# Kernel tuning notes

Hardware: AMD Instinct MI355X
Metric: run time of the kernel (lower is better)

## Reference

```python
import jax, jax.numpy as jnp
import numpy as np
from jax import lax

B, C, H, W = 64, 512, 20, 15
N = H * W  # must be 300 (ChannelAttention dim)
EPS = 1e-5


def layernorm(x, w, b):
    m = x.mean(-1, keepdims=True)
    v = x.var(-1, keepdims=True)
    return (x - m) * lax.rsqrt(v + EPS) * w + b


def batchnorm(x, w, b):  # training-mode BN over (B,H,W), x: (B,C,H,W)
    m = x.mean((0, 2, 3), keepdims=True)
    v = x.var((0, 2, 3), keepdims=True)
    return (x - m) * lax.rsqrt(v + EPS) * w[None, :, None, None] + b[None, :, None, None]


def cross_linear_attn(x1, x2, kv1_w, kv2_w, heads):
    # x: (B, n, c); kv_w: (2c, c). Linear-attention variant: softmax over channel axis of k^T v.
    b, n, c = x1.shape
    d = c // heads
    scale = d ** -0.5

    def split_q(x):
        return x.reshape(b, n, heads, d).transpose(0, 2, 1, 3)  # (b,h,n,d)

    def kv(x, w):
        t = (x @ w.T).reshape(b, n, 2, heads, d).transpose(2, 0, 3, 1, 4)
        return t[0], t[1]  # each (b,h,n,d)

    q1, q2 = split_q(x1), split_q(x2)
    k1, v1 = kv(x1, kv1_w)
    k2, v2 = kv(x2, kv2_w)

    def ctx(k, v):  # (b,h,d,d), softmax over dim -2
        return jax.nn.softmax(jnp.einsum('bhnd,bhne->bhde', k, v) * scale, axis=-2)

    c1, c2 = ctx(k1, v1), ctx(k2, v2)

    def out(q, cx):
        return jnp.einsum('bhnd,bhde->bhne', q, cx).transpose(0, 2, 1, 3).reshape(b, n, c)

    return out(q1, c2), out(q2, c1)  # cross: q1 uses ctx2, q2 uses ctx1


def conv1x1(x, w):  # x: (B,Ci,H,W), w: (Co,Ci)
    return jnp.einsum('oi,bihw->bohw', w, x)


def setup_inputs() -> dict:
    key = jax.random.key(0)
    ks = jax.random.split(key, 24)
    g = lambda i, shape, s=0.02: jax.random.normal(ks[i], shape, jnp.float32) * s
    inp = {
        'x1': jax.random.normal(ks[0], (B, C, H, W), jnp.float32),
        'x2': jax.random.normal(ks[1], (B, C, H, W), jnp.float32),
        # CrossPath channel_proj1/2: Linear(C, 2C) + LayerNorm(2C)
        'cp1_w': g(2, (2 * C, C)), 'cp1_b': jnp.zeros((2 * C,), jnp.float32),
        'ln1_w': jnp.ones((2 * C,), jnp.float32), 'ln1_b': jnp.zeros((2 * C,), jnp.float32),
        'cp2_w': g(3, (2 * C, C)), 'cp2_b': jnp.zeros((2 * C,), jnp.float32),
        'ln2_w': jnp.ones((2 * C,), jnp.float32), 'ln2_b': jnp.zeros((2 * C,), jnp.float32),
        # SpatialAttention (dim=C, heads=8) kv linears, no bias
        's_kv1_w': g(4, (2 * C, C)), 's_kv2_w': g(5, (2 * C, C)),
        # ChannelAttention (dim=N=300, heads=4) kv linears, no bias
        'c_kv1_w': g(6, (2 * N, N)), 'c_kv2_w': g(7, (2 * N, N)),
        # ChannelEmbed(2C -> C)
        'res_w': g(8, (C, 2 * C), np.sqrt(2.0 / C)),
        'ce1_w': g(9, (C, 2 * C), np.sqrt(2.0 / C)), 'ce1_b': jnp.zeros((C,), jnp.float32),
        'dw_w': g(10, (C, 1, 3, 3), np.sqrt(2.0 / 9.0)), 'dw_b': jnp.zeros((C,), jnp.float32),
        'ce3_w': g(11, (C, C), np.sqrt(2.0 / C)), 'ce3_b': jnp.zeros((C,), jnp.float32),
        'bn_e_w': jnp.ones((C,), jnp.float32), 'bn_e_b': jnp.zeros((C,), jnp.float32),
        'bn_o_w': jnp.ones((C,), jnp.float32), 'bn_o_b': jnp.zeros((C,), jnp.float32),
    }
    return inp


def reference(x1, x2, cp1_w, cp1_b, ln1_w, ln1_b, cp2_w, cp2_b, ln2_w, ln2_b,
              s_kv1_w, s_kv2_w, c_kv1_w, c_kv2_w,
              res_w, ce1_w, ce1_b, dw_w, dw_b, ce3_w, ce3_b,
              bn_e_w, bn_e_b, bn_o_w, bn_o_b):
    b, c, h, w = x1.shape
    n = h * w
    t1 = x1.reshape(b, c, n).transpose(0, 2, 1)  # (B,N,C)
    t2 = x2.reshape(b, c, n).transpose(0, 2, 1)

    a1 = jax.nn.relu(layernorm(t1 @ cp1_w.T + cp1_b, ln1_w, ln1_b))
    a2 = jax.nn.relu(layernorm(t2 @ cp2_w.T + cp2_b, ln2_w, ln2_b))
    c1, s1 = a1[..., :c], a1[..., c:]
    c2, s2 = a2[..., :c], a2[..., c:]

    v1, v2 = cross_linear_attn(s1, s2, s_kv1_w, s_kv2_w, heads=8)
    z1, z2 = cross_linear_attn(c1.transpose(0, 2, 1), c2.transpose(0, 2, 1),
                               c_kv1_w, c_kv2_w, heads=4)
    s = v1 + v2                                  # (B,N,C)
    cc = (z1 + z2).transpose(0, 2, 1)            # (B,N,C)

    merge = jnp.concatenate([s, cc], axis=-1)    # (B,N,2C)
    xm = merge.transpose(0, 2, 1).reshape(b, 2 * c, h, w)

    residual = conv1x1(xm, res_w)
    e = conv1x1(xm, ce1_w) + ce1_b[None, :, None, None]
    e = lax.conv_general_dilated(e, dw_w, (1, 1), 'SAME',
                                 dimension_numbers=('NCHW', 'OIHW', 'NCHW'),
                                 feature_group_count=c) + dw_b[None, :, None, None]
    e = jnp.where(e >= 0, e, 0.01 * e)  # LeakyReLU(0.01)
    e = conv1x1(e, ce3_w) + ce3_b[None, :, None, None]
    e = batchnorm(e, bn_e_w, bn_e_b)
    return batchnorm(residual + e, bn_o_w, bn_o_b)
```

## Files before the change

kernel.cpp:

```cpp
#include <hip/hip_runtime.h>

typedef unsigned short u16;
typedef __attribute__((ext_vector_type(8))) short bh8;
typedef __attribute__((ext_vector_type(4))) float f4;

__device__ __forceinline__ u16 f2b(float f){
  unsigned int u = __float_as_uint(f);
  u += 0x7fffu + ((u >> 16) & 1u);
  return (u16)(u >> 16);
}
__device__ __forceinline__ float b2f(u16 h){
  return __uint_as_float(((unsigned int)h) << 16);
}
__device__ __forceinline__ void gl16(const u16* g, u16* l){
  __builtin_amdgcn_global_load_lds((const __attribute__((address_space(1))) void*)g,
                                   (__attribute__((address_space(3))) void*)l, 16, 0, 0);
}

__global__ void pack_plain(const float* __restrict__ src, u16* __restrict__ dst, int count){
  int i = blockIdx.x*256 + threadIdx.x;
  if (i < count) dst[i] = f2b(src[i]);
}
__global__ void pack_ckv_k(const float* __restrict__ src, u16* __restrict__ dst){
  int i = blockIdx.x*256 + threadIdx.x;
  int nn = i / 320, kk = i - (i/320)*320;
  int t_ = (nn >= 320) ? 1 : 0;
  int rem = nn - t_*320;
  int hh = rem / 80, dd = rem - hh*80;
  int kh = kk / 80, kd = kk - kh*80;
  float v = 0.f;
  if (dd < 75 && kd < 75)
    v = src[(size_t)(t_*300 + hh*75 + dd)*300 + (kh*75 + kd)];
  dst[i] = f2b(v);
}
__global__ void pack_dw(const float* __restrict__ src, u16* __restrict__ dst){
  int i = blockIdx.x*256 + threadIdx.x;
  if (i < 4608){
    int t = i >> 9, c = i & 511;
    dst[i] = f2b(src[c*9 + t]);
  }
}
__global__ void pad_zero(u16* __restrict__ slack){
  const int j = blockIdx.x*256 + threadIdx.x;
  if (j < 2048) slack[j] = 0;
}

__global__ __launch_bounds__(256)
void transpose_k(const float* __restrict__ x, u16* __restrict__ t)
{
  __shared__ float tile[32][33];
  const int n0 = blockIdx.x * 32, c0 = blockIdx.y * 32, b = blockIdx.z;
  const int ln = threadIdx.x & 31, lr = threadIdx.x >> 5;
  #pragma unroll
  for (int q = 0; q < 4; q++) {
    const int c = c0 + lr + q*8, n = n0 + ln;
    tile[lr + q*8][ln] = (n < 300) ? x[((long)b*512 + c)*300 + n] : 0.f;
  }
  __syncthreads();
  #pragma unroll
  for (int q = 0; q < 4; q++) {
    const int n = n0 + lr + q*8;
    if (n < 300) t[((long)b*300 + n)*512 + c0 + ln] = f2b(tile[ln][lr + q*8]);
  }
}

template<int OUTF, int HASB>
__global__ __launch_bounds__(256)
void gemm_k(const u16* __restrict__ A, int lda,
            const u16* __restrict__ Bw, int ldb,
            u16* __restrict__ Cb, float* __restrict__ Cf, int ldc,
            const float* __restrict__ bias, int K)
{
  __shared__ u16 As[2][4096];
  __shared__ u16 Bs[2][4096];
  const int tid = threadIdx.x;
  const int gx = gridDim.x;
  const int nwg = gx * gridDim.y;
  const int flat = blockIdx.y * gx + blockIdx.x;
  const int newid = (flat & 7) * (nwg >> 3) + (flat >> 3);
  const long n0 = (long)(newid % gx) * 128;
  const long m0 = (long)(newid / gx) * 128;
  const int wave = tid >> 6, lane = tid & 63;
  const int l15 = lane & 15, lg = lane >> 4;
  const int wr = (wave >> 1) * 64, wc = (wave & 1) * 64;
  const int arow = tid >> 2;
  const int aseg = (((tid & 3) ^ ((arow >> 1) & 3))) * 8;
  const u16* Ag0 = A + (m0 + arow) * (long)lda + aseg;
  const u16* Ag1 = Ag0 + 64L * lda;
  const u16* Bg0 = Bw + (n0 + arow) * (long)ldb + aseg;
  const u16* Bg1 = Bg0 + 64L * ldb;
  const int to8 = tid * 8;
  int roA[4], roB[4];
  #pragma unroll
  for (int i = 0; i < 4; i++){
    const int rA = wr + i*16 + l15;
    roA[i] = rA*32 + ((lg ^ ((rA >> 1) & 3)) * 8);
    const int rB = wc + i*16 + l15;
    roB[i] = rB*32 + ((lg ^ ((rB >> 1) & 3)) * 8);
  }
  f4 acc[4][4] = {};
  const int NT = K >> 5;
  gl16(Ag0, &As[0][to8]); gl16(Ag1, &As[0][2048 + to8]);
  gl16(Bg0, &Bs[0][to8]); gl16(Bg1, &Bs[0][2048 + to8]);
  __syncthreads();
  int cur = 0;
  for (int t = 0; t < NT - 1; t++) {
    const int kt = (t + 1) << 5;
    const int nb = cur ^ 1;
    gl16(Ag0 + kt, &As[nb][to8]); gl16(Ag1 + kt, &As[nb][2048 + to8]);
    gl16(Bg0 + kt, &Bs[nb][to8]); gl16(Bg1 + kt, &Bs[nb][2048 + to8]);
    bh8 af[4], bf[4];
    #pragma unroll
    for (int mi = 0; mi < 4; mi++) af[mi] = *(const bh8*)&As[cur][roA[mi]];
    #pragma unroll
    for (int ni = 0; ni < 4; ni++) bf[ni] = *(const bh8*)&Bs[cur][roB[ni]];
    #pragma unroll
    for (int mi = 0; mi < 4; mi++)
      #pragma unroll
      for (int ni = 0; ni < 4; ni++)
        acc[mi][ni] = __builtin_amdgcn_mfma_f32_16x16x32_bf16(af[mi], bf[ni], acc[mi][ni], 0, 0, 0);
    __syncthreads();
    cur = nb;
  }
  {
    bh8 af[4], bf[4];
    #pragma unroll
    for (int mi = 0; mi < 4; mi++) af[mi] = *(const bh8*)&As[cur][roA[mi]];
    #pragma unroll
    for (int ni = 0; ni < 4; ni++) bf[ni] = *(const bh8*)&Bs[cur][roB[ni]];
    #pragma unroll
    for (int mi = 0; mi < 4; mi++)
      #pragma unroll
      for (int ni = 0; ni < 4; ni++)
        acc[mi][ni] = __builtin_amdgcn_mfma_f32_16x16x32_bf16(af[mi], bf[ni], acc[mi][ni], 0, 0, 0);
  }
  if (OUTF == 2) {
    if (n0 < 512) {
      #pragma unroll
      for (int ni = 0; ni < 4; ni++) {
        const long cn = n0 + wc + ni*16 + l15;
        #pragma unroll
        for (int mi = 0; mi < 4; mi++)
          #pragma unroll
          for (int r = 0; r < 4; r++) {
            const long cm = m0 + wr + mi*16 + lg*4 + r;
            Cf[cm * ldc + cn] = acc[mi][ni][r];
          }
      }
    } else {
      #pragma unroll
      for (int ni = 0; ni < 4; ni++) {
        const long cn = n0 - 512 + wc + ni*16 + l15;
        const float bv = bias[cn];
        #pragma unroll
        for (int mi = 0; mi < 4; mi++)
          #pragma unroll
          for (int r = 0; r < 4; r++) {
            const long cm = m0 + wr + mi*16 + lg*4 + r;
            Cb[cm * ldc + cn] = f2b(acc[mi][ni][r] + bv);
          }
      }
    }
  } else {
    #pragma unroll
    for (int ni = 0; ni < 4; ni++) {
      const long cn = n0 + wc + ni*16 + l15;
      const float bv = HASB ? bias[cn] : 0.0f;
      #pragma unroll
      for (int mi = 0; mi < 4; mi++) {
        #pragma unroll
        for (int r = 0; r < 4; r++) {
          const long cm = m0 + wr + mi*16 + lg*4 + r;
          const float v = acc[mi][ni][r] + bv;
          if (OUTF) Cf[cm * ldc + cn] = v;
          else      Cb[cm * ldc + cn] = f2b(v);
        }
      }
    }
  }
}

__global__ __launch_bounds__(256)
void ln_kernel(const u16* __restrict__ apre, const float* __restrict__ lw, const float* __restrict__ lb,
               u16* __restrict__ s, u16* __restrict__ cT)
{
  __shared__ u16 tile[40][520];
  const int bh = blockIdx.x;
  const int b = bh >> 2, h = bh & 3;
  const int z = blockIdx.y;
  const int dd0 = z ? 40 : 0;
  const int ndd = z ? 35 : 40;
  const int segbase = z ? 5 : 0;
  const int tid = threadIdx.x, w = tid >> 6, lane = tid & 63;
  const int r0 = b*300 + h*75 + dd0;
  for (int dl = w; dl < ndd; dl += 4){
    const int r = r0 + dl;
    const u16* row = apre + (size_t)r*1024 + lane*8;
    const bh8 vc = *(const bh8*)row;
    const bh8 vs = *(const bh8*)(row + 512);
    float fc[8], fs[8];
    float sm = 0.f, sq = 0.f;
    #pragma unroll
    for (int j = 0; j < 8; j++){
      fc[j] = b2f((u16)vc[j]); fs[j] = b2f((u16)vs[j]);
      sm += fc[j] + fs[j];
      sq += fc[j]*fc[j] + fs[j]*fs[j];
    }
    #pragma unroll
    for (int o = 32; o; o >>= 1){ sm += __shfl_xor(sm, o); sq += __shfl_xor(sq, o); }
    const float mean = sm * (1.f/1024.f);
    const float rstd = rsqrtf(sq*(1.f/1024.f) - mean*mean + 1e-5f);
    bh8 oc, os;
    #pragma unroll
    for (int j = 0; j < 8; j++){
      const int c = lane*8 + j;
      const float y1 = (fc[j]-mean)*rstd*lw[c] + lb[c];
      oc[j] = (short)f2b(fmaxf(y1, 0.f));
      const float y2 = (fs[j]-mean)*rstd*lw[512+c] + lb[512+c];
      os[j] = (short)f2b(fmaxf(y2, 0.f));
    }
    *(bh8*)&tile[dl][lane*8] = oc;
    *(bh8*)&s[(size_t)r*512 + lane*8] = os;
  }
  __syncthreads();
  for (int i = tid; i < 2560; i += 256){
    const int c = i / 5, sg = i - (i/5)*5;
    const int seg = segbase + sg;
    bh8 ov;
    #pragma unroll
    for (int j = 0; j < 8; j++){
      const int dl = seg*8 + j - dd0;
      ov[j] = (short)((dl >= 0 && dl < ndd) ? tile[dl][c] : (u16)0);
    }
    *(bh8*)&cT[((size_t)b*512 + c)*320 + h*80 + seg*8] = ov;
  }
}

template<int D, int DREAL, int OS>
__global__ __launch_bounds__(256)
void ctx_kernel(const u16* __restrict__ kva, const u16* __restrict__ kvb,
                u16* __restrict__ outp, int K, int RS, int VOFF, float scale)
{
  constexpr int NT = D/16, MT = D/16, MTL = (MT+3)/4, SEG = D/8;
  __shared__ u16 vT[D][40];
  __shared__ u16 kT[D][40];
  const int h = blockIdx.x, b = blockIdx.y, iq = blockIdx.z;
  const int Hn = gridDim.x;
  const u16* base = (iq ? kvb : kva) + (size_t)b*K*RS + h*D;
  u16* out = outp + (((size_t)iq*64 + b)*Hn + h)*(size_t)(D*OS);
  const int tid = threadIdx.x, w = tid >> 6, lane = tid & 63, l15 = lane & 15, lg = lane >> 4;
  f4 acc[MTL][NT] = {};
  for (int k0 = 0; k0 < K; k0 += 32) {
    __syncthreads();
    for (int sI = tid; sI < 32*SEG; sI += 256) {
      const int nn = sI / SEG, dseg = sI - (sI/SEG)*SEG;
      bh8 kk = {}, vv = {};
      const int krow = k0 + nn;
      if (krow < K) {
        const u16* p = base + (size_t)krow*RS + dseg*8;
        kk = *(const bh8*)p;
        vv = *(const bh8*)(p + VOFF);
      }
      #pragma unroll
      for (int j = 0; j < 8; j++){
        kT[dseg*8+j][nn] = (u16)kk[j];
        vT[dseg*8+j][nn] = (u16)vv[j];
      }
    }
    __syncthreads();
    #pragma unroll
    for (int ii = 0; ii < MTL; ii++){
      const int mt = w + ii*4;
      if (MT % 4 != 0 && mt >= MT) break;
      const bh8 a = *(const bh8*)&vT[mt*16 + l15][lg*8];
      #pragma unroll
      for (int nt = 0; nt < NT; nt++){
        const bh8 bb = *(const bh8*)&kT[nt*16 + l15][lg*8];
        acc[ii][nt] = __builtin_amdgcn_mfma_f32_16x16x32_bf16(a, bb, acc[ii][nt], 0, 0, 0);
      }
    }
  }
  #pragma unroll
  for (int ii = 0; ii < MTL; ii++){
    const int mt = w + ii*4;
    if (MT % 4 != 0 && mt >= MT) continue;
    #pragma unroll
    for (int r = 0; r < 4; r++){
      const int e = mt*16 + lg*4 + r;
      float xs[NT]; float mx = -1e30f;
      #pragma unroll
      for (int nt = 0; nt < NT; nt++){
        float x = acc[ii][nt][r] * scale;
        if (DREAL != D && (nt*16 + l15) >= DREAL) x = -1e30f;
        xs[nt] = x; mx = fmaxf(mx, x);
      }
      mx = fmaxf(mx, __shfl_xor(mx,1)); mx = fmaxf(mx, __shfl_xor(mx,2));
      mx = fmaxf(mx, __shfl_xor(mx,4)); mx = fmaxf(mx, __shfl_xor(mx,8));
      float smv = 0.f;
      #pragma unroll
      for (int nt = 0; nt < NT; nt++){
        const float p = (xs[nt] > -1e29f) ? __expf(xs[nt]-mx) : 0.f;
        xs[nt] = p; smv += p;
      }
      smv += __shfl_xor(smv,1); smv += __shfl_xor(smv,2);
      smv += __shfl_xor(smv,4); smv += __shfl_xor(smv,8);
      const float inv = 1.f / smv;
      #pragma unroll
      for (int nt = 0; nt < NT; nt++)
        out[(size_t)e*OS + nt*16 + l15] = f2b(xs[nt]*inv);
      if (OS > D) out[(size_t)e*OS + D + l15] = 0;
    }
  }
}

__global__ __launch_bounds__(256)
void sp_out_kernel(const u16* __restrict__ s1, const u16* __restrict__ s2,
                   const u16* __restrict__ csT, u16* __restrict__ merge)
{
  const int h = blockIdx.x, b = blockIdx.y;
  const int tid = threadIdx.x, w = tid >> 6, lane = tid & 63, l15 = lane & 15, lg = lane >> 4;
  const u16* c1 = csT + (((size_t)b)*8 + h)*4096;
  const u16* c2 = csT + (((size_t)64 + b)*8 + h)*4096;
  for (int mt = w; mt < 19; mt += 4) {
    const int m = mt*16 + l15;
    const bool mv = (m < 300);
    const u16* q1 = s1 + ((size_t)b*300 + m)*512 + h*64;
    const u16* q2 = s2 + ((size_t)b*300 + m)*512 + h*64;
    f4 acc[4] = {};
    #pragma unroll
    for (int kc = 0; kc < 2; kc++){
      bh8 a1 = {}, a2 = {};
      if (mv){ a1 = *(const bh8*)(q1 + kc*32 + lg*8); a2 = *(const bh8*)(q2 + kc*32 + lg*8); }
      #pragma unroll
      for (int nt = 0; nt < 4; nt++){
        const bh8 b2v = *(const bh8*)&c2[(size_t)(nt*16+l15)*64 + kc*32 + lg*8];
        acc[nt] = __builtin_amdgcn_mfma_f32_16x16x32_bf16(a1, b2v, acc[nt], 0, 0, 0);
        const bh8 b1v = *(const bh8*)&c1[(size_t)(nt*16+l15)*64 + kc*32 + lg*8];
        acc[nt] = __builtin_amdgcn_mfma_f32_16x16x32_bf16(a2, b1v, acc[nt], 0, 0, 0);
      }
    }
    #pragma unroll
    for (int nt = 0; nt < 4; nt++)
      #pragma unroll
      for (int r = 0; r < 4; r++){
        const int mm = mt*16 + lg*4 + r;
        if (mm < 300)
          merge[((size_t)b*300 + mm)*1024 + h*64 + nt*16 + l15] = f2b(acc[nt][r]);
      }
  }
}

__global__ __launch_bounds__(256)
void ch_out_kernel(const u16* __restrict__ cT1, const u16* __restrict__ cT2,
                   const u16* __restrict__ ccT, u16* __restrict__ merge)
{
  const int cb = blockIdx.x, h = blockIdx.y, b = blockIdx.z;
  const int tid = threadIdx.x, w = tid >> 6, lane = tid & 63, l15 = lane & 15, lg = lane >> 4;
  const int chbase = cb*128 + w*32;
  f4 acc[5][2] = {};
  #pragma unroll
  for (int oi = 0; oi < 2; oi++){
    const u16* Am = ccT + (((size_t)((oi==0)?1:0)*64 + b)*4 + h)*(size_t)(80*96);
    const u16* qb = (oi==0) ? cT1 : cT2;
    #pragma unroll
    for (int kc = 0; kc < 3; kc++){
      bh8 bf[2];
      #pragma unroll
      for (int nf = 0; nf < 2; nf++){
        const int ch = chbase + nf*16 + l15;
        bf[nf] = *(const bh8*)&qb[((size_t)b*512 + ch)*320 + h*80 + kc*32 + lg*8];
      }
      #pragma unroll
      for (int mt = 0; mt < 5; mt++){
        const bh8 a = *(const bh8*)&Am[(size_t)(mt*16+l15)*96 + kc*32 + lg*8];
        #pragma unroll
        for (int nf = 0; nf < 2; nf++)
          acc[mt][nf] = __builtin_amdgcn_mfma_f32_16x16x32_bf16(a, bf[nf], acc[mt][nf], 0, 0, 0);
      }
    }
  }
  #pragma unroll
  for (int mt = 0; mt < 5; mt++)
    #pragma unroll
    for (int nf = 0; nf < 2; nf++)
      #pragma unroll
      for (int r = 0; r < 4; r++){
        const int e = mt*16 + lg*4 + r;
        if (e < 75)
          merge[((size_t)b*300 + h*75 + e)*1024 + 512 + chbase + nf*16 + l15] = f2b(acc[mt][nf][r]);
      }
}

__global__ __launch_bounds__(256)
void dw_kernel(const u16* __restrict__ e1, const u16* __restrict__ dwt,
               const float* __restrict__ bias, u16* __restrict__ d1)
{
  const int idx = blockIdx.x*256 + threadIdx.x;
  const int cg = idx & 63;
  const int sp = (idx >> 6) % 300;
  const int b  = idx / (64*300);
  const int c0 = cg*8;
  const int hh = sp / 15, ww = sp - hh*15;
  float acc[8];
  {
    const float4 b0 = *(const float4*)&bias[c0];
    const float4 b1 = *(const float4*)&bias[c0+4];
    acc[0]=b0.x; acc[1]=b0.y; acc[2]=b0.z; acc[3]=b0.w;
    acc[4]=b1.x; acc[5]=b1.y; acc[6]=b1.z; acc[7]=b1.w;
  }
  #pragma unroll
  for (int dy = -1; dy <= 1; dy++){
    const int h2 = hh + dy; if (h2 < 0 || h2 >= 20) continue;
    #pragma unroll
    for (int dx = -1; dx <= 1; dx++){
      const int w2 = ww + dx; if (w2 < 0 || w2 >= 15) continue;
      const bh8 vv = *(const bh8*)&e1[((size_t)b*300 + h2*15 + w2)*512 + c0];
      const int t = (dy+1)*3 + (dx+1);
      const bh8 wv = *(const bh8*)&dwt[t*512 + c0];
      #pragma unroll
      for (int j = 0; j < 8; j++)
        acc[j] += b2f((u16)vv[j]) * b2f((u16)wv[j]);
    }
  }
  bh8 ov;
  #pragma unroll
  for (int j = 0; j < 8; j++){
    float y = acc[j];
    y = (y >= 0.f) ? y : 0.01f*y;
    ov[j] = (short)f2b(y);
  }
  *(bh8*)&d1[((size_t)b*300 + sp)*512 + c0] = ov;
}

__global__ __launch_bounds__(256)
void stats_e(const float* __restrict__ e3, float* __restrict__ st){
  const int tid = threadIdx.x;
  const int c0 = tid*2;
  const size_t r0 = (size_t)blockIdx.x * 128;
  float s0=0,s1=0,q0=0,q1=0;
  for (int rr = 0; rr < 128; rr++){
    const float2 v = *(const float2*)&e3[(r0+rr)*512 + c0];
    s0 += v.x; s1 += v.y; q0 += v.x*v.x; q1 += v.y*v.y;
  }
  atomicAdd(&st[c0], s0); atomicAdd(&st[c0+1], s1);
  atomicAdd(&st[512+c0], q0); atomicAdd(&st[512+c0+1], q1);
}
__global__ void fin_e(float* st, const float* __restrict__ w, const float* __restrict__ b){
  const int c = threadIdx.x;
  const float m = st[c] * (1.f/19200.f);
  const float v = st[512+c] * (1.f/19200.f) - m*m;
  const float a = w[c] * rsqrtf(v + 1e-5f);
  st[1024+c] = a; st[1536+c] = b[c] - m*a;
}
__global__ __launch_bounds__(256)
void stats_o(const float* __restrict__ res, const float* __restrict__ e3, float* __restrict__ st){
  const int tid = threadIdx.x;
  const int c0 = tid*2;
  const float a0 = st[1024+c0], b0v = st[1536+c0];
  const float a1 = st[1024+c0+1], b1v = st[1536+c0+1];
  const size_t r0 = (size_t)blockIdx.x * 128;
  float s0=0,s1=0,q0=0,q1=0;
  for (int rr = 0; rr < 128; rr++){
    const size_t o2 = (r0+rr)*512 + c0;
    const float2 rv = *(const float2*)&res[o2];
    const float2 ev = *(const float2*)&e3[o2];
    const float v0 = rv.x + ev.x*a0 + b0v;
    const float v1 = rv.y + ev.y*a1 + b1v;
    s0 += v0; s1 += v1; q0 += v0*v0; q1 += v1*v1;
  }
  atomicAdd(&st[2048+c0], s0); atomicAdd(&st[2048+c0+1], s1);
  atomicAdd(&st[2560+c0], q0); atomicAdd(&st[2560+c0+1], q1);
}
__global__ void fin_o(float* st, const float* __restrict__ w, const float* __restrict__ b){
  const int c = threadIdx.x;
  const float m = st[2048+c] * (1.f/19200.f);
  const float v = st[2560+c] * (1.f/19200.f) - m*m;
  const float a = w[c] * rsqrtf(v + 1e-5f);
  st[3072+c] = a; st[3584+c] = b[c] - m*a;
}
__global__ __launch_bounds__(256)
void final_kernel(const float* __restrict__ res, const float* __restrict__ e3,
                  const float* __restrict__ st, float* __restrict__ outp)
{
  __shared__ float tile[64][65];
  const int spt = blockIdx.x, cht = blockIdx.y, b = blockIdx.z;
  const int tid = threadIdx.x;
  const int sp0 = spt*64, ch0 = cht*64;
  for (int idx = tid; idx < 4096; idx += 256){
    const int cl = idx & 63, sl = idx >> 6;
    const int sp = sp0 + sl;
    float v = 0.f;
    if (sp < 300){
      const size_t off = ((size_t)b*300 + sp)*512 + ch0 + cl;
      const int c = ch0 + cl;
      const float e = e3[off]*st[1024+c] + st[1536+c];
      v = (res[off] + e)*st[3072+c] + st[3584+c];
    }
    tile[sl][cl] = v;
  }
  __syncthreads();
  for (int idx = tid; idx < 4096; idx += 256){
    const int sl = idx & 63, cl = idx >> 6;
    const int sp = sp0 + sl;
    if (sp < 300)
      outp[((size_t)b*512 + ch0 + cl)*300 + sp] = tile[sl][cl];
  }
}

extern "C" void kernel_launch(void* const* d_in, const int* in_sizes, int n_in,
                              void* d_out, int out_size, void* d_ws, size_t ws_size,
                              hipStream_t stream)
{
  const float* x1    = (const float*)d_in[0];
  const float* x2    = (const float*)d_in[1];
  const float* cp1_w = (const float*)d_in[2];
  const float* cp1_b = (const float*)d_in[3];
  const float* ln1_w = (const float*)d_in[4];
  const float* ln1_b = (const float*)d_in[5];
  const float* cp2_w = (const float*)d_in[6];
  const float* cp2_b = (const float*)d_in[7];
  const float* ln2_w = (const float*)d_in[8];
  const float* ln2_b = (const float*)d_in[9];
  const float* skv1w = (const float*)d_in[10];
  const float* skv2w = (const float*)d_in[11];
  const float* ckv1w = (const float*)d_in[12];
  const float* ckv2w = (const float*)d_in[13];
  const float* resw  = (const float*)d_in[14];
  const float* ce1w  = (const float*)d_in[15];
  const float* ce1b  = (const float*)d_in[16];
  const float* dww   = (const float*)d_in[17];
  const float* dwb   = (const float*)d_in[18];
  const float* ce3w  = (const float*)d_in[19];
  const float* ce3b  = (const float*)d_in[20];
  const float* bnew  = (const float*)d_in[21];
  const float* bneb  = (const float*)d_in[22];
  const float* bnow  = (const float*)d_in[23];
  const float* bnob  = (const float*)d_in[24];
  float* out = (float*)d_out;
  char* ws = (char*)d_ws;

  const size_t SZ_T    = (size_t)19200*512*2;
  const size_t SZ_APRE = (size_t)19200*1024*2;
  const size_t SZ_CKV  = (size_t)32768*640*2;
  const size_t SZ_CT   = (size_t)64*512*320*2;
  const size_t SZ_F32  = (size_t)19200*512*4;

  size_t off = 0;
  auto AL = [&](size_t sz){ size_t r = off; off += (sz + 255) & ~(size_t)255; return r; };
  const size_t oR0 = AL(2*SZ_T);
  const size_t oR1 = AL(2*SZ_CKV);
  const size_t oR2 = AL(2*SZ_T);
  const size_t oR3 = AL(2*SZ_CT + 4096);
  const size_t oR4 = AL(SZ_F32);
  const size_t oR5 = AL((size_t)2*64*8*64*64*2);
  const size_t oR6 = AL((size_t)2*64*4*80*96*2);
  const size_t oWcp1  = AL((size_t)1024*512*2);
  const size_t oWcp2  = AL((size_t)1024*512*2);
  const size_t oWskv1 = AL((size_t)1024*512*2);
  const size_t oWskv2 = AL((size_t)1024*512*2);
  const size_t oWckv1 = AL((size_t)640*320*2);
  const size_t oWckv2 = AL((size_t)640*320*2);
  const size_t oWresce = AL((size_t)1024*1024*2);
  const size_t oWce3  = AL((size_t)512*512*2);
  const size_t oWdw   = AL((size_t)9*512*2);
  const size_t oST    = AL(16384);
  (void)ws_size; (void)in_sizes; (void)n_in; (void)out_size;

  u16* t1    = (u16*)(ws + oR0);
  u16* t2    = (u16*)(ws + oR0 + SZ_T);
  u16* merge = (u16*)(ws + oR0);
  u16* apre1 = (u16*)(ws + oR1);
  u16* apre2 = (u16*)(ws + oR1 + SZ_APRE);
  u16* kv1   = apre1;
  u16* kv2   = apre2;
  u16* ckv1  = (u16*)(ws + oR1);
  u16* ckv2  = (u16*)(ws + oR1 + SZ_CKV);
  u16* s1    = (u16*)(ws + oR2);
  u16* s2    = (u16*)(ws + oR2 + SZ_T);
  u16* e1    = s1;
  u16* d1    = s2;
  u16* cT1   = (u16*)(ws + oR3);
  u16* cT2   = (u16*)(ws + oR3 + SZ_CT);
  u16* slack = (u16*)(ws + oR3 + 2*SZ_CT);
  float* e3  = (float*)(ws + oR3);
  float* resb = (float*)(ws + oR4);
  u16* csT   = (u16*)(ws + oR5);
  u16* ccT   = (u16*)(ws + oR6);
  u16* wcp1  = (u16*)(ws + oWcp1);
  u16* wcp2  = (u16*)(ws + oWcp2);
  u16* wskv1 = (u16*)(ws + oWskv1);
  u16* wskv2 = (u16*)(ws + oWskv2);
  u16* wckv1 = (u16*)(ws + oWckv1);
  u16* wckv2 = (u16*)(ws + oWckv2);
  u16* wresce = (u16*)(ws + oWresce);
  u16* wce3  = (u16*)(ws + oWce3);
  u16* wdw   = (u16*)(ws + oWdw);
  float* st  = (float*)(ws + oST);

  hipMemsetAsync(st, 0, 16384, stream);
  pad_zero<<<8,256,0,stream>>>(slack);
  pack_plain<<<2048,256,0,stream>>>(cp1_w, wcp1, 524288);
  pack_plain<<<2048,256,0,stream>>>(cp2_w, wcp2, 524288);
  pack_plain<<<2048,256,0,stream>>>(skv1w, wskv1, 524288);
  pack_plain<<<2048,256,0,stream>>>(skv2w, wskv2, 524288);
  pack_ckv_k<<<800,256,0,stream>>>(ckv1w, wckv1);
  pack_ckv_k<<<800,256,0,stream>>>(ckv2w, wckv2);
  pack_plain<<<2048,256,0,stream>>>(resw, wresce, 524288);
  pack_plain<<<2048,256,0,stream>>>(ce1w, wresce + 524288, 524288);
  pack_plain<<<1024,256,0,stream>>>(ce3w, wce3, 262144);
  pack_dw<<<18,256,0,stream>>>(dww, wdw);

  transpose_k<<<dim3(10,16,64),256,0,stream>>>(x1, t1);
  transpose_k<<<dim3(10,16,64),256,0,stream>>>(x2, t2);

  gemm_k<0,1><<<dim3(8,150),256,0,stream>>>(t1,512, wcp1,512, apre1,nullptr,1024, cp1_b, 512);
  gemm_k<0,1><<<dim3(8,150),256,0,stream>>>(t2,512, wcp2,512, apre2,nullptr,1024, cp2_b, 512);

  ln_kernel<<<dim3(256,2),256,0,stream>>>(apre1, ln1_w, ln1_b, s1, cT1);
  ln_kernel<<<dim3(256,2),256,0,stream>>>(apre2, ln2_w, ln2_b, s2, cT2);

  gemm_k<0,0><<<dim3(8,150),256,0,stream>>>(s1,512, wskv1,512, kv1,nullptr,1024, nullptr, 512);
  gemm_k<0,0><<<dim3(8,150),256,0,stream>>>(s2,512, wskv2,512, kv2,nullptr,1024, nullptr, 512);

  ctx_kernel<64,64,64><<<dim3(8,64,2),256,0,stream>>>(kv1, kv2, csT, 300, 1024, 512, 0.125f);

  gemm_k<0,0><<<dim3(5,256),256,0,stream>>>(cT1,320, wckv1,320, ckv1,nullptr,640, nullptr, 320);
  gemm_k<0,0><<<dim3(5,256),256,0,stream>>>(cT2,320, wckv2,320, ckv2,nullptr,640, nullptr, 320);

  ctx_kernel<80,75,96><<<dim3(4,64,2),256,0,stream>>>(ckv1, ckv2, ccT, 512, 640, 320, 0.115470054f);

  sp_out_kernel<<<dim3(8,64),256,0,stream>>>(s1, s2, csT, merge);
  ch_out_kernel<<<dim3(4,4,64),256,0,stream>>>(cT1, cT2, ccT, merge);

  gemm_k<2,0><<<dim3(8,150),256,0,stream>>>(merge,1024, wresce,1024, e1, resb, 512, ce1b, 1024);

  dw_kernel<<<4800,256,0,stream>>>(e1, wdw, dwb, d1);

  gemm_k<1,1><<<dim3(4,150),256,0,stream>>>(d1,512, wce3,512, nullptr,e3,512, ce3b, 512);

  stats_e<<<150,256,0,stream>>>(e3, st);
  fin_e<<<1,512,0,stream>>>(st, bnew, bneb);
  stats_o<<<150,256,0,stream>>>(resb, e3, st);
  fin_o<<<1,512,0,stream>>>(st, bnow, bnob);
  final_kernel<<<dim3(5,8,64),256,0,stream>>>(resb, e3, st, out);
}
```

Measured before the change: 597.5 us.

## Triple-buffer GEMM loads, batch paired GEMMs, and fuse the two batchnorm statistics passes

The GEMM kernel moves from a double-buffered to a triple-buffered LDS pipeline with explicit vmcnt waits and raw barriers, keeping two tiles in flight. Paired GEMMs for the two branches are merged into single launches that pick the second weight and bias by row half. The two batchnorm statistics passes are combined into one pass that gathers sums, squares and cross products of e3 and the residual, and the output BN moments are derived algebraically. This trades more LDS per block, and so possibly lower occupancy, for fewer launches and one fewer read of e3 and the residual. Computing variance from expanded moments may lose some precision.

```diff
diff --git a/kernel.cpp b/kernel.cpp
--- a/kernel.cpp
+++ b/kernel.cpp
@@ -67,12 +67,12 @@
 template<int OUTF, int HASB>
 __global__ __launch_bounds__(256)
 void gemm_k(const u16* __restrict__ A, int lda,
-            const u16* __restrict__ Bw, int ldb,
+            const u16* __restrict__ Bw, const u16* __restrict__ Bw2, int ldb, long mhalf,
             u16* __restrict__ Cb, float* __restrict__ Cf, int ldc,
-            const float* __restrict__ bias, int K)
-{
-  __shared__ u16 As[2][4096];
-  __shared__ u16 Bs[2][4096];
+            const float* __restrict__ bias, const float* __restrict__ bias2, int K)
+{
+  __shared__ u16 As[3][4096];
+  __shared__ u16 Bs[3][4096];
   const int tid = threadIdx.x;
   const int gx = gridDim.x;
   const int nwg = gx * gridDim.y;
@@ -80,6 +80,8 @@
   const int newid = (flat & 7) * (nwg >> 3) + (flat >> 3);
   const long n0 = (long)(newid % gx) * 128;
   const long m0 = (long)(newid / gx) * 128;
+  const u16* Bwp = Bw; const float* bp = bias;
+  if (Bw2 != nullptr && m0 >= mhalf){ Bwp = Bw2; bp = bias2; }
   const int wave = tid >> 6, lane = tid & 63;
   const int l15 = lane & 15, lg = lane >> 4;
   const int wr = (wave >> 1) * 64, wc = (wave & 1) * 64;
@@ -87,7 +89,7 @@
   const int aseg = (((tid & 3) ^ ((arow >> 1) & 3))) * 8;
   const u16* Ag0 = A + (m0 + arow) * (long)lda + aseg;
   const u16* Ag1 = Ag0 + 64L * lda;
-  const u16* Bg0 = Bw + (n0 + arow) * (long)ldb + aseg;
+  const u16* Bg0 = Bwp + (n0 + arow) * (long)ldb + aseg;
   const u16* Bg1 = Bg0 + 64L * ldb;
   const int to8 = tid * 8;
   int roA[4], roB[4];
@@ -100,39 +102,36 @@
   }
   f4 acc[4][4] = {};
   const int NT = K >> 5;
-  gl16(Ag0, &As[0][to8]); gl16(Ag1, &As[0][2048 + to8]);
-  gl16(Bg0, &Bs[0][to8]); gl16(Bg1, &Bs[0][2048 + to8]);
-  __syncthreads();
-  int cur = 0;
-  for (int t = 0; t < NT - 1; t++) {
-    const int kt = (t + 1) << 5;
-    const int nb = cur ^ 1;
-    gl16(Ag0 + kt, &As[nb][to8]); gl16(Ag1 + kt, &As[nb][2048 + to8]);
-    gl16(Bg0 + kt, &Bs[nb][to8]); gl16(Bg1 + kt, &Bs[nb][2048 + to8]);
+  {
+    gl16(Ag0, &As[0][to8]); gl16(Ag1, &As[0][2048 + to8]);
+    gl16(Bg0, &Bs[0][to8]); gl16(Bg1, &Bs[0][2048 + to8]);
+    gl16(Ag0 + 32, &As[1][to8]); gl16(Ag1 + 32, &As[1][2048 + to8]);
+    gl16(Bg0 + 32, &Bs[1][to8]); gl16(Bg1 + 32, &Bs[1][2048 + to8]);
+  }
+  int rd = 0;
+  for (int t = 0; t < NT; t++) {
+    if (t < NT - 1) { asm volatile("s_waitcnt vmcnt(4)" ::: "memory"); }
+    else            { asm volatile("s_waitcnt vmcnt(0)" ::: "memory"); }
+    __builtin_amdgcn_sched_barrier(0);
+    __builtin_amdgcn_s_barrier();
+    __builtin_amdgcn_sched_barrier(0);
+    if (t + 2 < NT) {
+      int wb = rd + 2; if (wb >= 3) wb -= 3;
+      const int kt = (t + 2) << 5;
+      gl16(Ag0 + kt, &As[wb][to8]); gl16(Ag1 + kt, &As[wb][2048 + to8]);
+      gl16(Bg0 + kt, &Bs[wb][to8]); gl16(Bg1 + kt, &Bs[wb][2048 + to8]);
+    }
     bh8 af[4], bf[4];
     #pragma unroll
-    for (int mi = 0; mi < 4; mi++) af[mi] = *(const bh8*)&As[cur][roA[mi]];
-    #pragma unroll
-    for (int ni = 0; ni < 4; ni++) bf[ni] = *(const bh8*)&Bs[cur][roB[ni]];
+    for (int mi = 0; mi < 4; mi++) af[mi] = *(const bh8*)&As[rd][roA[mi]];
+    #pragma unroll
+    for (int ni = 0; ni < 4; ni++) bf[ni] = *(const bh8*)&Bs[rd][roB[ni]];
     #pragma unroll
     for (int mi = 0; mi < 4; mi++)
       #pragma unroll
       for (int ni = 0; ni < 4; ni++)
         acc[mi][ni] = __builtin_amdgcn_mfma_f32_16x16x32_bf16(af[mi], bf[ni], acc[mi][ni], 0, 0, 0);
-    __syncthreads();
-    cur = nb;
-  }
-  {
-    bh8 af[4], bf[4];
-    #pragma unroll
-    for (int mi = 0; mi < 4; mi++) af[mi] = *(const bh8*)&As[cur][roA[mi]];
-    #pragma unroll
-    for (int ni = 0; ni < 4; ni++) bf[ni] = *(const bh8*)&Bs[cur][roB[ni]];
-    #pragma unroll
-    for (int mi = 0; mi < 4; mi++)
-      #pragma unroll
-      for (int ni = 0; ni < 4; ni++)
-        acc[mi][ni] = __builtin_amdgcn_mfma_f32_16x16x32_bf16(af[mi], bf[ni], acc[mi][ni], 0, 0, 0);
+    rd++; if (rd == 3) rd = 0;
   }
   if (OUTF == 2) {
     if (n0 < 512) {
@@ -165,7 +164,7 @@
     #pragma unroll
     for (int ni = 0; ni < 4; ni++) {
       const long cn = n0 + wc + ni*16 + l15;
-      const float bv = HASB ? bias[cn] : 0.0f;
+      const float bv = HASB ? bp[cn] : 0.0f;
       #pragma unroll
       for (int mi = 0; mi < 4; mi++) {
         #pragma unroll
@@ -433,50 +432,41 @@
 }
 
 __global__ __launch_bounds__(256)
-void stats_e(const float* __restrict__ e3, float* __restrict__ st){
+void stats_k(const float* __restrict__ e3, const float* __restrict__ res, float* __restrict__ st){
   const int tid = threadIdx.x;
   const int c0 = tid*2;
   const size_t r0 = (size_t)blockIdx.x * 128;
-  float s0=0,s1=0,q0=0,q1=0;
-  for (int rr = 0; rr < 128; rr++){
-    const float2 v = *(const float2*)&e3[(r0+rr)*512 + c0];
-    s0 += v.x; s1 += v.y; q0 += v.x*v.x; q1 += v.y*v.y;
-  }
-  atomicAdd(&st[c0], s0); atomicAdd(&st[c0+1], s1);
-  atomicAdd(&st[512+c0], q0); atomicAdd(&st[512+c0+1], q1);
-}
-__global__ void fin_e(float* st, const float* __restrict__ w, const float* __restrict__ b){
-  const int c = threadIdx.x;
-  const float m = st[c] * (1.f/19200.f);
-  const float v = st[512+c] * (1.f/19200.f) - m*m;
-  const float a = w[c] * rsqrtf(v + 1e-5f);
-  st[1024+c] = a; st[1536+c] = b[c] - m*a;
-}
-__global__ __launch_bounds__(256)
-void stats_o(const float* __restrict__ res, const float* __restrict__ e3, float* __restrict__ st){
-  const int tid = threadIdx.x;
-  const int c0 = tid*2;
-  const float a0 = st[1024+c0], b0v = st[1536+c0];
-  const float a1 = st[1024+c0+1], b1v = st[1536+c0+1];
-  const size_t r0 = (size_t)blockIdx.x * 128;
-  float s0=0,s1=0,q0=0,q1=0;
+  float se0=0,se1=0,qe0=0,qe1=0,sr0=0,sr1=0,qr0=0,qr1=0,x0=0,x1=0;
   for (int rr = 0; rr < 128; rr++){
     const size_t o2 = (r0+rr)*512 + c0;
+    const float2 ev = *(const float2*)&e3[o2];
     const float2 rv = *(const float2*)&res[o2];
-    const float2 ev = *(const float2*)&e3[o2];
-    const float v0 = rv.x + ev.x*a0 + b0v;
-    const float v1 = rv.y + ev.y*a1 + b1v;
-    s0 += v0; s1 += v1; q0 += v0*v0; q1 += v1*v1;
-  }
-  atomicAdd(&st[2048+c0], s0); atomicAdd(&st[2048+c0+1], s1);
-  atomicAdd(&st[2560+c0], q0); atomicAdd(&st[2560+c0+1], q1);
-}
-__global__ void fin_o(float* st, const float* __restrict__ w, const float* __restrict__ b){
+    se0 += ev.x; se1 += ev.y; qe0 += ev.x*ev.x; qe1 += ev.y*ev.y;
+    sr0 += rv.x; sr1 += rv.y; qr0 += rv.x*rv.x; qr1 += rv.y*rv.y;
+    x0  += ev.x*rv.x; x1 += ev.y*rv.y;
+  }
+  atomicAdd(&st[c0], se0);      atomicAdd(&st[c0+1], se1);
+  atomicAdd(&st[512+c0], qe0);  atomicAdd(&st[512+c0+1], qe1);
+  atomicAdd(&st[1024+c0], sr0); atomicAdd(&st[1024+c0+1], sr1);
+  atomicAdd(&st[1536+c0], qr0); atomicAdd(&st[1536+c0+1], qr1);
+  atomicAdd(&st[2048+c0], x0);  atomicAdd(&st[2048+c0+1], x1);
+}
+__global__ void fin_k(float* st, const float* __restrict__ we, const float* __restrict__ be,
+                      const float* __restrict__ wo, const float* __restrict__ bo){
   const int c = threadIdx.x;
-  const float m = st[2048+c] * (1.f/19200.f);
-  const float v = st[2560+c] * (1.f/19200.f) - m*m;
-  const float a = w[c] * rsqrtf(v + 1e-5f);
-  st[3072+c] = a; st[3584+c] = b[c] - m*a;
+  const float Nf = 19200.f, iN = 1.f/19200.f;
+  const float Se = st[c], Qe = st[512+c], Sr = st[1024+c], Qr = st[1536+c], X = st[2048+c];
+  const float me = Se*iN;
+  const float ve = Qe*iN - me*me;
+  const float ae = we[c]*rsqrtf(ve + 1e-5f);
+  const float bev = be[c] - me*ae;
+  const float So = Sr + ae*Se + Nf*bev;
+  const float Qo = Qr + ae*ae*Qe + Nf*bev*bev + 2.f*ae*X + 2.f*bev*Sr + 2.f*ae*bev*Se;
+  const float mo = So*iN;
+  const float vo = Qo*iN - mo*mo;
+  const float ao = wo[c]*rsqrtf(vo + 1e-5f);
+  const float bov = bo[c] - mo*ao;
+  st[2560+c] = ae; st[3072+c] = bev; st[3584+c] = ao; st[4096+c] = bov;
 }
 __global__ __launch_bounds__(256)
 void final_kernel(const float* __restrict__ res, const float* __restrict__ e3,
@@ -493,8 +483,8 @@
     if (sp < 300){
       const size_t off = ((size_t)b*300 + sp)*512 + ch0 + cl;
       const int c = ch0 + cl;
-      const float e = e3[off]*st[1024+c] + st[1536+c];
-      v = (res[off] + e)*st[3072+c] + st[3584+c];
+      const float e = e3[off]*st[2560+c] + st[3072+c];
+      v = (res[off] + e)*st[3584+c] + st[4096+c];
     }
     tile[sl][cl] = v;
   }
@@ -563,18 +553,13 @@
   const size_t oWresce = AL((size_t)1024*1024*2);
   const size_t oWce3  = AL((size_t)512*512*2);
   const size_t oWdw   = AL((size_t)9*512*2);
-  const size_t oST    = AL(16384);
+  const size_t oST    = AL(20480);
   (void)ws_size; (void)in_sizes; (void)n_in; (void)out_size;
 
   u16* t1    = (u16*)(ws + oR0);
-  u16* t2    = (u16*)(ws + oR0 + SZ_T);
   u16* merge = (u16*)(ws + oR0);
   u16* apre1 = (u16*)(ws + oR1);
-  u16* apre2 = (u16*)(ws + oR1 + SZ_APRE);
-  u16* kv1   = apre1;
-  u16* kv2   = apre2;
   u16* ckv1  = (u16*)(ws + oR1);
-  u16* ckv2  = (u16*)(ws + oR1 + SZ_CKV);
   u16* s1    = (u16*)(ws + oR2);
   u16* s2    = (u16*)(ws + oR2 + SZ_T);
   u16* e1    = s1;
@@ -597,7 +582,11 @@
   u16* wdw   = (u16*)(ws + oWdw);
   float* st  = (float*)(ws + oST);
 
-  hipMemsetAsync(st, 0, 16384, stream);
+  u16* t2    = t1 + 19200*512;
+  u16* kv1   = apre1;
+  u16* ckv2  = ckv1 + (size_t)32768*640;
+
+  hipMemsetAsync(st, 0, 10240, stream);
   pad_zero<<<8,256,0,stream>>>(slack);
   pack_plain<<<2048,256,0,stream>>>(cp1_w, wcp1, 524288);
   pack_plain<<<2048,256,0,stream>>>(cp2_w, wcp2, 524288);
@@ -613,34 +602,34 @@
   transpose_k<<<dim3(10,16,64),256,0,stream>>>(x1, t1);
   transpose_k<<<dim3(10,16,64),256,0,stream>>>(x2, t2);
 
-  gemm_k<0,1><<<dim3(8,150),256,0,stream>>>(t1,512, wcp1,512, apre1,nullptr,1024, cp1_b, 512);
-  gemm_k<0,1><<<dim3(8,150),256,0,stream>>>(t2,512, wcp2,512, apre2,nullptr,1024, cp2_b, 512);
+  gemm_k<0,1><<<dim3(8,300),256,0,stream>>>(t1,512, wcp1,wcp2,512, 19200L,
+                                            apre1,nullptr,1024, cp1_b,cp2_b, 512);
 
   ln_kernel<<<dim3(256,2),256,0,stream>>>(apre1, ln1_w, ln1_b, s1, cT1);
-  ln_kernel<<<dim3(256,2),256,0,stream>>>(apre2, ln2_w, ln2_b, s2, cT2);
-
-  gemm_k<0,0><<<dim3(8,150),256,0,stream>>>(s1,512, wskv1,512, kv1,nullptr,1024, nullptr, 512);
-  gemm_k<0,0><<<dim3(8,150),256,0,stream>>>(s2,512, wskv2,512, kv2,nullptr,1024, nullptr, 512);
-
-  ctx_kernel<64,64,64><<<dim3(8,64,2),256,0,stream>>>(kv1, kv2, csT, 300, 1024, 512, 0.125f);
-
-  gemm_k<0,0><<<dim3(5,256),256,0,stream>>>(cT1,320, wckv1,320, ckv1,nullptr,640, nullptr, 320);
-  gemm_k<0,0><<<dim3(5,256),256,0,stream>>>(cT2,320, wckv2,320, ckv2,nullptr,640, nullptr, 320);
+  ln_kernel<<<dim3(256,2),256,0,stream>>>(apre1 + (size_t)19200*1024, ln2_w, ln2_b, s2, cT2);
+
+  gemm_k<0,0><<<dim3(8,300),256,0,stream>>>(s1,512, wskv1,wskv2,512, 19200L,
+                                            kv1,nullptr,1024, nullptr,nullptr, 512);
+
+  ctx_kernel<64,64,64><<<dim3(8,64,2),256,0,stream>>>(kv1, kv1 + (size_t)19200*1024, csT, 300, 1024, 512, 0.125f);
+
+  gemm_k<0,0><<<dim3(5,512),256,0,stream>>>(cT1,320, wckv1,wckv2,320, 32768L,
+                                            ckv1,nullptr,640, nullptr,nullptr, 320);
 
   ctx_kernel<80,75,96><<<dim3(4,64,2),256,0,stream>>>(ckv1, ckv2, ccT, 512, 640, 320, 0.115470054f);
 
   sp_out_kernel<<<dim3(8,64),256,0,stream>>>(s1, s2, csT, merge);
   ch_out_kernel<<<dim3(4,4,64),256,0,stream>>>(cT1, cT2, ccT, merge);
 
-  gemm_k<2,0><<<dim3(8,150),256,0,stream>>>(merge,1024, wresce,1024, e1, resb, 512, ce1b, 1024);
+  gemm_k<2,0><<<dim3(8,150),256,0,stream>>>(merge,1024, wresce,nullptr,1024, (long)1<<40,
+                                            e1, resb, 512, ce1b,nullptr, 1024);
 
   dw_kernel<<<4800,256,0,stream>>>(e1, wdw, dwb, d1);
 
-  gemm_k<1,1><<<dim3(4,150),256,0,stream>>>(d1,512, wce3,512, nullptr,e3,512, ce3b, 512);
-
-  stats_e<<<150,256,0,stream>>>(e3, st);
-  fin_e<<<1,512,0,stream>>>(st, bnew, bneb);
-  stats_o<<<150,256,0,stream>>>(resb, e3, st);
-  fin_o<<<1,512,0,stream>>>(st, bnow, bnob);
+  gemm_k<1,1><<<dim3(4,150),256,0,stream>>>(d1,512, wce3,nullptr,512, (long)1<<40,
+                                            nullptr,e3,512, ce3b,nullptr, 512);
+
+  stats_k<<<150,256,0,stream>>>(e3, resb, st);
+  fin_k<<<1,512,0,stream>>>(st, bnew, bneb, bnow, bnob);
   final_kernel<<<dim3(5,8,64),256,0,stream>>>(resb, e3, st, out);
 }
```

After: 547.1 us. 8.4% less time.
